# Optimization experiments

Hardware: AMD Instinct MI355X
Metric: run time of the kernel (lower is better)

The kernel has to match this reference:

```python
import jax, jax.numpy as jnp
import numpy as np

B, S, DIM, NH = 2, 2048, 1024, 8
DH = DIM // NH
GATE_SOFT_CAP = 15.0
BACKEND_EPS = 5e-05
NORM_EPS = 1e-06


def setup_inputs() -> dict:
    key = jax.random.key(0)
    kq, kk, kv, kw = jax.random.split(key, 4)
    q = jax.random.normal(kq, (B, S, DIM), dtype=jnp.float32)
    k = jax.random.normal(kk, (B, S, DIM), dtype=jnp.float32)
    v = jax.random.normal(kv, (B, S, DIM), dtype=jnp.float32)
    # ifgate: Linear(3*dim, 2*num_heads). Init weight is zeros in the module;
    # use small random weights so the gate path is non-trivial.
    ifgate_w = 0.02 * jax.random.normal(kw, (2 * NH, 3 * DIM), dtype=jnp.float32)
    # bias per reset_parameters: i_bias = -10, f_bias = linspace(3, 6, NH)
    ifgate_b = jnp.concatenate([
        jnp.full((NH,), -10.0, dtype=jnp.float32),
        jnp.linspace(3.0, 6.0, NH, dtype=jnp.float32),
    ])
    # residual-weight RMSNorm gain: effective gain = 1 + outnorm_w (init zeros)
    outnorm_w = jnp.zeros((DIM,), dtype=jnp.float32)
    return {"q": q, "k": k, "v": v, "ifgate_w": ifgate_w,
            "ifgate_b": ifgate_b, "outnorm_w": outnorm_w}


def _mlstm_parallel(q, k, v, i_pre, f_pre):
    # q,k,v: (B,NH,S,DH); i_pre,f_pre: (B,NH,S). Native stabilized parallel mLSTM.
    log_fg = jax.nn.log_sigmoid(f_pre)                       # (B,NH,S)
    lf_cs = jnp.cumsum(log_fg, axis=-1)                      # (B,NH,S)
    lf = jnp.concatenate([jnp.zeros_like(lf_cs[..., :1]), lf_cs], axis=-1)  # (B,NH,S+1)
    # log_D[t, s] = sum_{j=s+1}^{t} log_fg[j] + i_pre[s]  for s <= t, else -inf
    log_d = lf[..., 1:, None] - lf[..., None, 1:] + i_pre[..., None, :]     # (B,NH,S,S)
    t_idx = jnp.arange(q.shape[2])
    mask = t_idx[:, None] >= t_idx[None, :]
    log_d = jnp.where(mask, log_d, -jnp.inf)
    m = jnp.max(log_d, axis=-1, keepdims=True)               # (B,NH,S,1)
    d_mat = jnp.exp(log_d - m)                               # stabilized decays
    scores = jnp.einsum("bhtd,bhsd->bhts", q, k) * (1.0 / np.sqrt(DH))
    s_mat = scores * d_mat                                   # (B,NH,S,S)
    denom = jnp.maximum(jnp.abs(jnp.sum(s_mat, axis=-1, keepdims=True)),
                        jnp.exp(-m)) + BACKEND_EPS
    return jnp.einsum("bhts,bhsd->bhtd", s_mat, v) / denom   # (B,NH,S,DH)


def reference(q, k, v, ifgate_w, ifgate_b, outnorm_w):
    b, s, dim = q.shape
    # gate preactivations from concatenated q,k,v with tanh soft cap
    gate_in = jnp.concatenate([q, k, v], axis=-1)            # (B,S,3*DIM)
    pre = gate_in @ ifgate_w.T + ifgate_b                    # (B,S,2*NH)
    pre = GATE_SOFT_CAP * jnp.tanh(pre / GATE_SOFT_CAP)
    i_pre = pre[..., :NH].transpose(0, 2, 1)                 # (B,NH,S)
    f_pre = pre[..., NH:].transpose(0, 2, 1)                 # (B,NH,S)
    # split heads
    qh = q.reshape(b, s, NH, DH).transpose(0, 2, 1, 3)
    kh = k.reshape(b, s, NH, DH).transpose(0, 2, 1, 3)
    vh = v.reshape(b, s, NH, DH).transpose(0, 2, 1, 3)
    h = _mlstm_parallel(qh, kh, vh, i_pre, f_pre)            # (B,NH,S,DH)
    # multi-head RMSNorm with residual gain (bias is unused in the module's forward)
    rrms = jax.lax.rsqrt(jnp.mean(h * h, axis=-1, keepdims=True) + NORM_EPS)
    gain = (1.0 + outnorm_w).reshape(1, NH, 1, DH)
    h = h * rrms * gain
    return h.transpose(0, 2, 1, 3).reshape(b, s, dim)
```

## Files before the change

kernel.cpp:

```cpp
#include <hip/hip_runtime.h>
#include <math.h>

#define BB 2
#define SS 2048
#define DIMM 1024
#define NHH 8
#define DHH 128

constexpr float GATE_CAP = 15.0f;
constexpr float B_EPS = 5e-5f;
constexpr float N_EPS = 1e-6f;
constexpr float K_IS = 0.08838834764831845f;

typedef _Float16 f16x8 __attribute__((ext_vector_type(8)));
typedef __fp16  h16x2 __attribute__((ext_vector_type(2)));
typedef float f32x4 __attribute__((ext_vector_type(4)));

union U8 { f16x8 v; h16x2 h[4]; unsigned int u[4]; };

__device__ inline unsigned short f2bf(float x) {
    unsigned u = __builtin_bit_cast(unsigned, x);
    unsigned r = (u + 0x7fff + ((u >> 16) & 1)) >> 16;
    return (unsigned short)r;
}
__device__ inline float bf2f(unsigned short s) {
    unsigned u = ((unsigned)s) << 16;
    return __builtin_bit_cast(float, u);
}

#define GLD_LDS16(gsrc, ldst)                                                   \
    __builtin_amdgcn_global_load_lds(                                           \
        (const __attribute__((address_space(1))) unsigned int*)(gsrc),          \
        (__attribute__((address_space(3))) unsigned int*)(ldst), 16, 0, 0)

__global__ __launch_bounds__(256) void gate_kernel(
    const float* __restrict__ q, const float* __restrict__ k, const float* __restrict__ v,
    const float* __restrict__ gw, const float* __restrict__ gb,
    float* __restrict__ i_pre, float* __restrict__ lfcs)
{
    __shared__ __align__(16) float xs[2][8][1024];

    const int tid = threadIdx.x;
    const int lane = tid & 63;
    const int wv = tid >> 6;
    const int bs0 = blockIdx.x * 8;

    const float* srcs[3] = {q, k, v};

    auto stage = [&](int buf, int i) {
        const char* src = (const char*)(srcs[i] + (size_t)bs0 * DIMM);
        #pragma unroll
        for (int j = 0; j < 8; ++j) {
            GLD_LDS16(src + j * 4096 + wv * 1024 + lane * 16,
                      (char*)&xs[buf][j][0] + wv * 1024 + lane * 16);
        }
    };

    float acc[8][4];
    #pragma unroll
    for (int r = 0; r < 8; ++r)
        #pragma unroll
        for (int o = 0; o < 4; ++o) acc[r][o] = 0.f;

    stage(0, 0);

    for (int i = 0; i < 3; ++i) {
        const int cur = i & 1;
        if (i < 2) {
            stage(cur ^ 1, i + 1);
            asm volatile("s_waitcnt vmcnt(8)" ::: "memory");
        } else {
            asm volatile("s_waitcnt vmcnt(0)" ::: "memory");
        }
        __builtin_amdgcn_s_barrier();
        __builtin_amdgcn_sched_barrier(0);

        const float* gwi = gw + (wv * 4) * 3 * DIMM + i * DIMM;
        #pragma unroll
        for (int step = 0; step < 4; ++step) {
            float4 w4[4];
            #pragma unroll
            for (int o = 0; o < 4; ++o)
                w4[o] = *(const float4*)&gwi[o * 3 * DIMM + step * 256 + lane * 4];
            #pragma unroll
            for (int r = 0; r < 8; ++r) {
                const float4 xv = *(const float4*)&xs[cur][r][step * 256 + lane * 4];
                #pragma unroll
                for (int o = 0; o < 4; ++o)
                    acc[r][o] += xv.x * w4[o].x + xv.y * w4[o].y
                               + xv.z * w4[o].z + xv.w * w4[o].w;
            }
        }
        __builtin_amdgcn_s_barrier();
    }

    #pragma unroll
    for (int r = 0; r < 8; ++r)
        #pragma unroll
        for (int o = 0; o < 4; ++o) {
            acc[r][o] += __shfl_xor(acc[r][o], 16);
            acc[r][o] += __shfl_xor(acc[r][o], 32);
        }

    float* scr = &xs[0][0][0];
    const int l16 = lane & 15;
    if (l16 == lane) {
        #pragma unroll
        for (int r = 0; r < 8; ++r) {
            float4 st = {acc[r][0], acc[r][1], acc[r][2], acc[r][3]};
            *(float4*)&scr[wv * 576 + l16 * 36 + r * 4] = st;
        }
    }
    __syncthreads();

    if (tid < 128) {
        const int row = tid & 7, o = tid >> 3;
        const float* base = &scr[(o >> 2) * 576 + row * 4 + (o & 3)];
        float s = 0.f;
        #pragma unroll
        for (int j = 0; j < 16; ++j) s += base[j * 36];
        float p = s + gb[o];
        p = GATE_CAP * tanhf(p / GATE_CAP);
        const int bs = bs0 + row;
        const int b = bs >> 11, s2 = bs & 2047;
        if (o < NHH) {
            i_pre[((size_t)b * NHH + o) * SS + s2] = p;
        } else {
            const int h = o - NHH;
            const float ls = (p >= 0.f) ? -log1pf(expf(-p)) : p - log1pf(expf(p));
            lfcs[((size_t)b * NHH + h) * SS + s2] = ls;
        }
    }
}

__global__ __launch_bounds__(256) void prep_kv(
    const float* __restrict__ k, const float* __restrict__ v,
    unsigned short* __restrict__ k16, unsigned short* __restrict__ v16)
{
    const int id = blockIdx.x;
    const int bh = id & 15;
    const int st = id >> 4;
    const int b = bh >> 3, h = bh & 7;
    const int tid = threadIdx.x;

    {
        const float* kp = k + ((size_t)b * SS + st * 64) * DIMM + h * DHH;
        char* kb_ = (char*)k16 + ((size_t)bh * SS + st * 64) * 256;
        #pragma unroll
        for (int j = 0; j < 8; ++j) {
            const int item = j * 256 + tid;
            const int s = item >> 5, dq = item & 31;
            float4 kx = *(const float4*)&kp[(size_t)s * DIMM + dq * 4];
            h16x2 p0 = __builtin_amdgcn_cvt_pkrtz(kx.x, kx.y);
            h16x2 p1 = __builtin_amdgcn_cvt_pkrtz(kx.z, kx.w);
            uint2 wd;
            wd.x = __builtin_bit_cast(unsigned int, p0);
            wd.y = __builtin_bit_cast(unsigned int, p1);
            *(uint2*)(kb_ + s * 256 + ((dq * 8) ^ ((s & 7) << 4))) = wd;
        }
    }

    {
        const int d2 = (tid & 63) * 2;
        const int kb = (tid >> 6) & 1;
        const int gq = tid >> 7;
        const float* vp = v + ((size_t)b * SS + st * 64 + kb * 32) * DIMM + h * DHH + d2;
        char* base = (char*)v16 + ((size_t)bh * 32 + st) * 16384;
        #pragma unroll
        for (int gg = 0; gg < 2; ++gg) {
            const int g = gq * 2 + gg;
            float2 e[8];
            #pragma unroll
            for (int j = 0; j < 8; ++j) {
                const int s = 16 * (j >> 2) + 4 * g + (j & 3);
                e[j] = *(const float2*)&vp[(size_t)s * DIMM];
            }
            U8 u0, u1;
            u0.h[0] = __builtin_amdgcn_cvt_pkrtz(e[0].x, e[1].x);
            u0.h[1] = __builtin_amdgcn_cvt_pkrtz(e[2].x, e[3].x);
            u0.h[2] = __builtin_amdgcn_cvt_pkrtz(e[4].x, e[5].x);
            u0.h[3] = __builtin_amdgcn_cvt_pkrtz(e[6].x, e[7].x);
            u1.h[0] = __builtin_amdgcn_cvt_pkrtz(e[0].y, e[1].y);
            u1.h[1] = __builtin_amdgcn_cvt_pkrtz(e[2].y, e[3].y);
            u1.h[2] = __builtin_amdgcn_cvt_pkrtz(e[4].y, e[5].y);
            u1.h[3] = __builtin_amdgcn_cvt_pkrtz(e[6].y, e[7].y);
            const int p0 = kb * 64 + g * 16;
            *(f16x8*)(base + d2 * 128       + (p0 ^ ((d2 & 7) << 4)))       = u0.v;
            *(f16x8*)(base + (d2 + 1) * 128 + (p0 ^ (((d2 + 1) & 7) << 4))) = u1.v;
        }
    }
}

__global__ __launch_bounds__(256) void scan_kernel(
    const float* __restrict__ i_pre,
    float* __restrict__ lfcs, float* __restrict__ mstab, float* __restrict__ aa)
{
    const int bh = blockIdx.x;
    const int tid = threadIdx.x;
    const int lane = tid & 63, wv = tid >> 6;
    const size_t base = (size_t)bh * SS + tid * 8;

    float x[8];
    {
        float4 a0 = *(const float4*)&lfcs[base];
        float4 a1 = *(const float4*)&lfcs[base + 4];
        x[0] = a0.x; x[1] = a0.y; x[2] = a0.z; x[3] = a0.w;
        x[4] = a1.x; x[5] = a1.y; x[6] = a1.z; x[7] = a1.w;
    }
    #pragma unroll
    for (int i = 1; i < 8; ++i) x[i] += x[i - 1];

    const float tot = x[7];
    float inc = tot;
    #pragma unroll
    for (int off = 1; off < 64; off <<= 1) {
        float n = __shfl_up(inc, off);
        if (lane >= off) inc += n;
    }
    const float exc = inc - tot;

    __shared__ float wt[4], wm[4];
    if (lane == 63) wt[wv] = inc;
    __syncthreads();
    float wpre = 0.f;
    for (int w = 0; w < 4; ++w) if (w < wv) wpre += wt[w];
    const float off0 = exc + wpre;
    #pragma unroll
    for (int i = 0; i < 8; ++i) x[i] += off0;
    {
        float4 s0 = {x[0], x[1], x[2], x[3]}, s1 = {x[4], x[5], x[6], x[7]};
        *(float4*)&lfcs[base] = s0;
        *(float4*)&lfcs[base + 4] = s1;
    }

    float g[8];
    {
        float4 i0 = *(const float4*)&i_pre[base];
        float4 i1 = *(const float4*)&i_pre[base + 4];
        g[0] = i0.x - x[0]; g[1] = i0.y - x[1]; g[2] = i0.z - x[2]; g[3] = i0.w - x[3];
        g[4] = i1.x - x[4]; g[5] = i1.y - x[5]; g[6] = i1.z - x[6]; g[7] = i1.w - x[7];
        float4 s0 = {g[0], g[1], g[2], g[3]}, s1 = {g[4], g[5], g[6], g[7]};
        *(float4*)&aa[base] = s0;
        *(float4*)&aa[base + 4] = s1;
    }
    float mg[8];
    mg[0] = g[0];
    #pragma unroll
    for (int i = 1; i < 8; ++i) mg[i] = fmaxf(mg[i - 1], g[i]);

    float minc = mg[7];
    #pragma unroll
    for (int off = 1; off < 64; off <<= 1) {
        float n = __shfl_up(minc, off);
        if (lane >= off) minc = fmaxf(minc, n);
    }
    float mexc = __shfl_up(minc, 1);
    if (lane == 0) mexc = -1e30f;
    if (lane == 63) wm[wv] = minc;
    __syncthreads();
    float wmpre = -1e30f;
    for (int w = 0; w < 4; ++w) if (w < wv) wmpre = fmaxf(wmpre, wm[w]);
    const float pm = fmaxf(mexc, wmpre);
    float4 s0, s1;
    s0.x = x[0] + fmaxf(pm, mg[0]); s0.y = x[1] + fmaxf(pm, mg[1]);
    s0.z = x[2] + fmaxf(pm, mg[2]); s0.w = x[3] + fmaxf(pm, mg[3]);
    s1.x = x[4] + fmaxf(pm, mg[4]); s1.y = x[5] + fmaxf(pm, mg[5]);
    s1.z = x[6] + fmaxf(pm, mg[6]); s1.w = x[7] + fmaxf(pm, mg[7]);
    *(float4*)&mstab[base] = s0;
    *(float4*)&mstab[base + 4] = s1;
}

__global__ __launch_bounds__(256, 2) void mlstm_splitk(
    const float* __restrict__ q,
    const unsigned short* __restrict__ k16, const unsigned short* __restrict__ v16,
    const float* __restrict__ lfcs, const float* __restrict__ aa,
    unsigned short* __restrict__ pnum, float* __restrict__ pden)
{
    __shared__ __align__(16) unsigned short kbuf[2][8192];
    __shared__ __align__(16) unsigned short vbuf[2][8192];

    const int tid = threadIdx.x;
    const int lane = tid & 63;
    const int wv = tid >> 6;
    const int g = lane >> 4;
    const int l16 = lane & 15;

    const int id = blockIdx.x;
    int bh, qq, chunk;
    if (id < 256) {
        bh = id & 15;
        const int j = id >> 4;
        if (j < 7)       { qq = 5 + j;               chunk = 0; }
        else if (j == 7) { qq = 11;                  chunk = 1; }
        else             { qq = 12 + ((j - 8) >> 1); chunk = (j - 8) & 1; }
    } else {
        const int e = id - 256;
        bh = e & 15;
        const int j = e >> 4;
        if (j < 5)       { qq = j;             chunk = 0; }
        else if (j < 10) { qq = 6 + (j - 5);   chunk = 1; }
        else             { qq = 12 + (j - 10); chunk = 2; }
    }
    const int b = bh >> 3, h = bh & 7;
    const int tw0 = qq * 128 + 32 * wv;

    const size_t bhS = (size_t)bh * SS;
    const float* qp = q + (size_t)b * SS * DIMM + h * DHH;
    const char* kg = (const char*)k16 + (size_t)bh * 524288;
    const char* vg = (const char*)v16 + (size_t)bh * 524288;

    f16x8 qf[2][4];
    float cdec[2];
    #pragma unroll
    for (int nt = 0; nt < 2; ++nt) {
        const int t = tw0 + 16 * nt + l16;
        cdec[nt] = lfcs[bhS + t];
        const float* qrow = qp + (size_t)t * DIMM;
        #pragma unroll
        for (int kb = 0; kb < 4; ++kb) {
            float4 x0 = *(const float4*)&qrow[kb * 32 + g * 8];
            float4 x1 = *(const float4*)&qrow[kb * 32 + g * 8 + 4];
            U8 uu;
            uu.h[0] = __builtin_amdgcn_cvt_pkrtz(x0.x, x0.y);
            uu.h[1] = __builtin_amdgcn_cvt_pkrtz(x0.z, x0.w);
            uu.h[2] = __builtin_amdgcn_cvt_pkrtz(x1.x, x1.y);
            uu.h[3] = __builtin_amdgcn_cvt_pkrtz(x1.z, x1.w);
            qf[nt][kb] = uu.v;
        }
    }

    f32x4 oacc[2][8];
    #pragma unroll
    for (int nt = 0; nt < 2; ++nt)
        #pragma unroll
        for (int mt = 0; mt < 8; ++mt)
            oacc[nt][mt] = (f32x4){0.f, 0.f, 0.f, 0.f};
    float dpart[2] = {0.f, 0.f};

    const int st0 = chunk * 12;
    const int st1m = 2 * qq + 1;
    const int st1 = (st0 + 11 < st1m) ? (st0 + 11) : st1m;

    auto stage = [&](int bi, int st) {
        const char* ksrc = kg + (size_t)st * 16384;
        const char* vsrc = vg + (size_t)st * 16384;
        #pragma unroll
        for (int j = 0; j < 4; ++j) {
            const int off = (j * 4 + wv) * 1024;
            GLD_LDS16(ksrc + off + lane * 16, (char*)&kbuf[bi][0] + off);
            GLD_LDS16(vsrc + off + lane * 16, (char*)&vbuf[bi][0] + off);
        }
    };

    stage(0, st0);

    for (int st = st0; st <= st1; ++st) {
        const int cur = (st - st0) & 1;
        if (st < st1) {
            stage(cur ^ 1, st + 1);
            asm volatile("s_waitcnt vmcnt(8)" ::: "memory");
        } else {
            asm volatile("s_waitcnt vmcnt(0)" ::: "memory");
        }
        __builtin_amdgcn_s_barrier();
        __builtin_amdgcn_sched_barrier(0);

        const int s0 = st * 64;
        const float* ap = aa + bhS + s0;
        f32x4 av[4];
        av[0] = *(const f32x4*)&ap[g * 4];
        av[1] = *(const f32x4*)&ap[16 + g * 4];
        av[2] = *(const f32x4*)&ap[32 + g * 4];
        av[3] = *(const f32x4*)&ap[48 + g * 4];

        f32x4 stacc[2][4];
        #pragma unroll
        for (int nt = 0; nt < 2; ++nt)
            #pragma unroll
            for (int ct = 0; ct < 4; ++ct)
                stacc[nt][ct] = (f32x4){0.f, 0.f, 0.f, 0.f};
        #pragma unroll
        for (int ct = 0; ct < 4; ++ct) {
            const int row = ct * 16 + l16;
            #pragma unroll
            for (int kb = 0; kb < 4; ++kb) {
                f16x8 kf = *(const f16x8*)((const char*)&kbuf[cur][0] +
                            ((row * 256 + kb * 64 + g * 16) ^ ((row & 7) << 4)));
                stacc[0][ct] = __builtin_amdgcn_mfma_f32_16x16x32_f16(kf, qf[0][kb], stacc[0][ct], 0, 0, 0);
                stacc[1][ct] = __builtin_amdgcn_mfma_f32_16x16x32_f16(kf, qf[1][kb], stacc[1][ct], 0, 0, 0);
            }
        }

        const bool diag = (st >= 2 * qq);
        #pragma unroll
        for (int nt = 0; nt < 2; ++nt) {
            float dsum = 0.f;
            const int t_idx = tw0 + nt * 16 + l16;
            #pragma unroll
            for (int ct = 0; ct < 4; ++ct) {
                #pragma unroll
                for (int i = 0; i < 4; ++i) {
                    const float e = K_IS * __expf(cdec[nt] + av[ct][i]);
                    float val = stacc[nt][ct][i] * e;
                    if (diag && (s0 + ct * 16 + g * 4 + i > t_idx)) val = 0.f;
                    dsum += val;
                    stacc[nt][ct][i] = val;
                }
            }
            dpart[nt] += dsum;
        }

        f16x8 pf[2][2];
        #pragma unroll
        for (int nt = 0; nt < 2; ++nt) {
            #pragma unroll
            for (int kb = 0; kb < 2; ++kb) {
                U8 uu;
                uu.h[0] = __builtin_amdgcn_cvt_pkrtz(stacc[nt][2 * kb][0],     stacc[nt][2 * kb][1]);
                uu.h[1] = __builtin_amdgcn_cvt_pkrtz(stacc[nt][2 * kb][2],     stacc[nt][2 * kb][3]);
                uu.h[2] = __builtin_amdgcn_cvt_pkrtz(stacc[nt][2 * kb + 1][0], stacc[nt][2 * kb + 1][1]);
                uu.h[3] = __builtin_amdgcn_cvt_pkrtz(stacc[nt][2 * kb + 1][2], stacc[nt][2 * kb + 1][3]);
                pf[nt][kb] = uu.v;
            }
        }

        #pragma unroll
        for (int mt = 0; mt < 8; ++mt) {
            const int dI = mt * 16 + l16;
            #pragma unroll
            for (int kb = 0; kb < 2; ++kb) {
                f16x8 vf = *(const f16x8*)((const char*)&vbuf[cur][0] +
                            dI * 128 + ((kb * 64 + g * 16) ^ ((dI & 7) << 4)));
                oacc[0][mt] = __builtin_amdgcn_mfma_f32_16x16x32_f16(vf, pf[0][kb], oacc[0][mt], 0, 0, 0);
                oacc[1][mt] = __builtin_amdgcn_mfma_f32_16x16x32_f16(vf, pf[1][kb], oacc[1][mt], 0, 0, 0);
            }
        }
        __builtin_amdgcn_sched_barrier(0);
        __builtin_amdgcn_s_barrier();
    }

    const int uoff = (qq < 6) ? qq : ((qq < 12) ? (6 + 2 * (qq - 6)) : (18 + 3 * (qq - 12)));
    const size_t cidx = (size_t)bh * 30 + uoff + chunk;
    #pragma unroll
    for (int nt = 0; nt < 2; ++nt) {
        float den = dpart[nt];
        den += __shfl_xor(den, 16);
        den += __shfl_xor(den, 32);
        const int row = wv * 32 + nt * 16 + l16;
        if (g == 0) pden[cidx * 128 + row] = den;
        #pragma unroll
        for (int mt = 0; mt < 8; ++mt) {
            ushort4 pk;
            pk.x = f2bf(oacc[nt][mt][0]);
            pk.y = f2bf(oacc[nt][mt][1]);
            pk.z = f2bf(oacc[nt][mt][2]);
            pk.w = f2bf(oacc[nt][mt][3]);
            *(ushort4*)&pnum[((cidx * 64 + wv * 16 + nt * 8 + mt) << 8) + lane * 4] = pk;
        }
    }
}

__global__ __launch_bounds__(256) void reduce_kernel(
    const unsigned short* __restrict__ pnum, const float* __restrict__ pden,
    const float* __restrict__ mstab, const float* __restrict__ onw,
    float* __restrict__ out)
{
    const int id = blockIdx.x;
    const int bh = id & 15;
    const int qq = id >> 4;
    const int b = bh >> 3, h = bh & 7;
    const int tid = threadIdx.x;
    const int lane = tid & 63;
    const int wv = tid >> 6;
    const int g = lane >> 4;
    const int l16 = lane & 15;

    const int nch = (qq < 6) ? 1 : ((qq < 12) ? 2 : 3);
    const int uoff = (qq < 6) ? qq : ((qq < 12) ? (6 + 2 * (qq - 6)) : (18 + 3 * (qq - 12)));
    const size_t cbase = (size_t)bh * 30 + uoff;

    f32x4 acc[2][8];
    #pragma unroll
    for (int nt = 0; nt < 2; ++nt)
        #pragma unroll
        for (int mt = 0; mt < 8; ++mt)
            acc[nt][mt] = (f32x4){0.f, 0.f, 0.f, 0.f};
    float den[2] = {0.f, 0.f};

    for (int c = 0; c < nch; ++c) {
        const size_t fb = (cbase + c) * 64 + wv * 16;
        #pragma unroll
        for (int nt = 0; nt < 2; ++nt) {
            #pragma unroll
            for (int mt = 0; mt < 8; ++mt) {
                ushort4 t4 = *(const ushort4*)&pnum[((fb + nt * 8 + mt) << 8) + lane * 4];
                acc[nt][mt][0] += bf2f(t4.x);
                acc[nt][mt][1] += bf2f(t4.y);
                acc[nt][mt][2] += bf2f(t4.z);
                acc[nt][mt][3] += bf2f(t4.w);
            }
            den[nt] += pden[(cbase + c) * 128 + wv * 32 + nt * 16 + l16];
        }
    }

    #pragma unroll
    for (int nt = 0; nt < 2; ++nt) {
        const int t = qq * 128 + wv * 32 + nt * 16 + l16;
        const float m = mstab[(size_t)bh * SS + t];
        const float em = __expf(-m);
        const float dt = den[nt] * em;
        const float denf = fmaxf(fabsf(dt), em) + B_EPS;
        const float inv = em / denf;
        float ssq = 0.f;
        #pragma unroll
        for (int mt = 0; mt < 8; ++mt) {
            #pragma unroll
            for (int i = 0; i < 4; ++i) {
                acc[nt][mt][i] *= inv;
                ssq += acc[nt][mt][i] * acc[nt][mt][i];
            }
        }
        ssq += __shfl_xor(ssq, 16);
        ssq += __shfl_xor(ssq, 32);
        const float rms = rsqrtf(ssq * (1.0f / DHH) + N_EPS);

        float* orow = out + ((size_t)b * SS + t) * DIMM + h * DHH;
        #pragma unroll
        for (int mt = 0; mt < 8; ++mt) {
            float4 gn = *(const float4*)&onw[h * DHH + mt * 16 + g * 4];
            float4 o4;
            o4.x = acc[nt][mt][0] * rms * (1.f + gn.x);
            o4.y = acc[nt][mt][1] * rms * (1.f + gn.y);
            o4.z = acc[nt][mt][2] * rms * (1.f + gn.z);
            o4.w = acc[nt][mt][3] * rms * (1.f + gn.w);
            *(float4*)&orow[mt * 16 + g * 4] = o4;
        }
    }
}

extern "C" void kernel_launch(void* const* d_in, const int* in_sizes, int n_in,
                              void* d_out, int out_size, void* d_ws, size_t ws_size,
                              hipStream_t stream) {
    const float* q   = (const float*)d_in[0];
    const float* k   = (const float*)d_in[1];
    const float* v   = (const float*)d_in[2];
    const float* gw  = (const float*)d_in[3];
    const float* gb  = (const float*)d_in[4];
    const float* onw = (const float*)d_in[5];
    float* out = (float*)d_out;

    float* ws    = (float*)d_ws;
    float* i_pre = ws;
    float* lfcs  = ws + 32768;
    float* mm    = ws + 65536;
    float* aa    = ws + 98304;
    float* pden  = ws + 131072;
    unsigned short* pnum = (unsigned short*)((char*)d_ws + 1048576);
    unsigned short* k16  = (unsigned short*)((char*)d_ws + 16777216);
    unsigned short* v16  = (unsigned short*)((char*)d_ws + 25165824);

    hipLaunchKernelGGL(gate_kernel, dim3(BB * SS / 8), dim3(256), 0, stream,
                       q, k, v, gw, gb, i_pre, lfcs);
    hipLaunchKernelGGL(prep_kv, dim3(16 * 32), dim3(256), 0, stream, k, v, k16, v16);
    hipLaunchKernelGGL(scan_kernel, dim3(BB * NHH), dim3(256), 0, stream, i_pre, lfcs, mm, aa);
    hipLaunchKernelGGL(mlstm_splitk, dim3(480), dim3(256), 0, stream,
                       q, k16, v16, lfcs, aa, pnum, pden);
    hipLaunchKernelGGL(reduce_kernel, dim3(16 * 16), dim3(256), 0, stream,
                       pnum, pden, mm, onw, out);
}
```

Baseline: 84.07 us.

## Fuse prep and scan kernels, interleave QK/PV MFMA phases, use exp2 decay

Merges the K/V fp16 conversion kernel and the gate scan kernel into one launch, with the extra blocks doing the scan, which removes one launch boundary. In the mLSTM split-K kernel, the QK^T, decay and PV stages are split into halves and interleaved, with s_setprio raised around the MFMA sections, so matrix and vector work can overlap. The decay exponent is precomputed in base-2 with the 1/sqrt(d) scale folded into the log, so exp2 replaces expf times a constant. The gate weights and the decay-vector loads are hoisted ahead of the barrier waits to hide their latency, at the cost of more live registers.

```diff
diff --git a/kernel.cpp b/kernel.cpp
--- a/kernel.cpp
+++ b/kernel.cpp
@@ -10,7 +10,8 @@
 constexpr float GATE_CAP = 15.0f;
 constexpr float B_EPS = 5e-5f;
 constexpr float N_EPS = 1e-6f;
-constexpr float K_IS = 0.08838834764831845f;
+constexpr float LOG2E = 1.4426950408889634f;
+constexpr float LN_KIS = -2.4260151319598084f;
 
 typedef _Float16 f16x8 __attribute__((ext_vector_type(8)));
 typedef __fp16  h16x2 __attribute__((ext_vector_type(2)));
@@ -66,6 +67,14 @@
 
     for (int i = 0; i < 3; ++i) {
         const int cur = i & 1;
+        const float* gwi = gw + (wv * 4) * 3 * DIMM + i * DIMM;
+        float4 w4[4][4];
+        #pragma unroll
+        for (int step = 0; step < 4; ++step)
+            #pragma unroll
+            for (int o = 0; o < 4; ++o)
+                w4[step][o] = *(const float4*)&gwi[o * 3 * DIMM + step * 256 + lane * 4];
+
         if (i < 2) {
             stage(cur ^ 1, i + 1);
             asm volatile("s_waitcnt vmcnt(8)" ::: "memory");
@@ -75,20 +84,15 @@
         __builtin_amdgcn_s_barrier();
         __builtin_amdgcn_sched_barrier(0);
 
-        const float* gwi = gw + (wv * 4) * 3 * DIMM + i * DIMM;
         #pragma unroll
         for (int step = 0; step < 4; ++step) {
-            float4 w4[4];
-            #pragma unroll
-            for (int o = 0; o < 4; ++o)
-                w4[o] = *(const float4*)&gwi[o * 3 * DIMM + step * 256 + lane * 4];
             #pragma unroll
             for (int r = 0; r < 8; ++r) {
                 const float4 xv = *(const float4*)&xs[cur][r][step * 256 + lane * 4];
                 #pragma unroll
                 for (int o = 0; o < 4; ++o)
-                    acc[r][o] += xv.x * w4[o].x + xv.y * w4[o].y
-                               + xv.z * w4[o].z + xv.w * w4[o].w;
+                    acc[r][o] += xv.x * w4[step][o].x + xv.y * w4[step][o].y
+                               + xv.z * w4[step][o].z + xv.w * w4[step][o].w;
             }
         }
         __builtin_amdgcn_s_barrier();
@@ -133,70 +137,70 @@
     }
 }
 
-__global__ __launch_bounds__(256) void prep_kv(
+__global__ __launch_bounds__(256) void prep_scan(
     const float* __restrict__ k, const float* __restrict__ v,
-    unsigned short* __restrict__ k16, unsigned short* __restrict__ v16)
-{
-    const int id = blockIdx.x;
-    const int bh = id & 15;
-    const int st = id >> 4;
-    const int b = bh >> 3, h = bh & 7;
-    const int tid = threadIdx.x;
-
-    {
-        const float* kp = k + ((size_t)b * SS + st * 64) * DIMM + h * DHH;
-        char* kb_ = (char*)k16 + ((size_t)bh * SS + st * 64) * 256;
-        #pragma unroll
-        for (int j = 0; j < 8; ++j) {
-            const int item = j * 256 + tid;
-            const int s = item >> 5, dq = item & 31;
-            float4 kx = *(const float4*)&kp[(size_t)s * DIMM + dq * 4];
-            h16x2 p0 = __builtin_amdgcn_cvt_pkrtz(kx.x, kx.y);
-            h16x2 p1 = __builtin_amdgcn_cvt_pkrtz(kx.z, kx.w);
-            uint2 wd;
-            wd.x = __builtin_bit_cast(unsigned int, p0);
-            wd.y = __builtin_bit_cast(unsigned int, p1);
-            *(uint2*)(kb_ + s * 256 + ((dq * 8) ^ ((s & 7) << 4))) = wd;
-        }
-    }
-
-    {
-        const int d2 = (tid & 63) * 2;
-        const int kb = (tid >> 6) & 1;
-        const int gq = tid >> 7;
-        const float* vp = v + ((size_t)b * SS + st * 64 + kb * 32) * DIMM + h * DHH + d2;
-        char* base = (char*)v16 + ((size_t)bh * 32 + st) * 16384;
-        #pragma unroll
-        for (int gg = 0; gg < 2; ++gg) {
-            const int g = gq * 2 + gg;
-            float2 e[8];
-            #pragma unroll
-            for (int j = 0; j < 8; ++j) {
-                const int s = 16 * (j >> 2) + 4 * g + (j & 3);
-                e[j] = *(const float2*)&vp[(size_t)s * DIMM];
-            }
-            U8 u0, u1;
-            u0.h[0] = __builtin_amdgcn_cvt_pkrtz(e[0].x, e[1].x);
-            u0.h[1] = __builtin_amdgcn_cvt_pkrtz(e[2].x, e[3].x);
-            u0.h[2] = __builtin_amdgcn_cvt_pkrtz(e[4].x, e[5].x);
-            u0.h[3] = __builtin_amdgcn_cvt_pkrtz(e[6].x, e[7].x);
-            u1.h[0] = __builtin_amdgcn_cvt_pkrtz(e[0].y, e[1].y);
-            u1.h[1] = __builtin_amdgcn_cvt_pkrtz(e[2].y, e[3].y);
-            u1.h[2] = __builtin_amdgcn_cvt_pkrtz(e[4].y, e[5].y);
-            u1.h[3] = __builtin_amdgcn_cvt_pkrtz(e[6].y, e[7].y);
-            const int p0 = kb * 64 + g * 16;
-            *(f16x8*)(base + d2 * 128       + (p0 ^ ((d2 & 7) << 4)))       = u0.v;
-            *(f16x8*)(base + (d2 + 1) * 128 + (p0 ^ (((d2 + 1) & 7) << 4))) = u1.v;
-        }
-    }
-}
-
-__global__ __launch_bounds__(256) void scan_kernel(
+    unsigned short* __restrict__ k16, unsigned short* __restrict__ v16,
     const float* __restrict__ i_pre,
     float* __restrict__ lfcs, float* __restrict__ mstab, float* __restrict__ aa)
 {
-    const int bh = blockIdx.x;
+    const int id = blockIdx.x;
     const int tid = threadIdx.x;
+    __shared__ float wt[4], wm[4];
+
+    if (id < 512) {
+        const int bh = id & 15;
+        const int st = id >> 4;
+        const int b = bh >> 3, h = bh & 7;
+
+        {
+            const float* kp = k + ((size_t)b * SS + st * 64) * DIMM + h * DHH;
+            char* kb_ = (char*)k16 + ((size_t)bh * SS + st * 64) * 256;
+            #pragma unroll
+            for (int j = 0; j < 8; ++j) {
+                const int item = j * 256 + tid;
+                const int s = item >> 5, dq = item & 31;
+                float4 kx = *(const float4*)&kp[(size_t)s * DIMM + dq * 4];
+                h16x2 p0 = __builtin_amdgcn_cvt_pkrtz(kx.x, kx.y);
+                h16x2 p1 = __builtin_amdgcn_cvt_pkrtz(kx.z, kx.w);
+                uint2 wd;
+                wd.x = __builtin_bit_cast(unsigned int, p0);
+                wd.y = __builtin_bit_cast(unsigned int, p1);
+                *(uint2*)(kb_ + s * 256 + ((dq * 8) ^ ((s & 7) << 4))) = wd;
+            }
+        }
+        {
+            const int d2 = (tid & 63) * 2;
+            const int kb = (tid >> 6) & 1;
+            const int gq = tid >> 7;
+            const float* vp = v + ((size_t)b * SS + st * 64 + kb * 32) * DIMM + h * DHH + d2;
+            char* base = (char*)v16 + ((size_t)bh * 32 + st) * 16384;
+            #pragma unroll
+            for (int gg = 0; gg < 2; ++gg) {
+                const int g = gq * 2 + gg;
+                float2 e[8];
+                #pragma unroll
+                for (int j = 0; j < 8; ++j) {
+                    const int s = 16 * (j >> 2) + 4 * g + (j & 3);
+                    e[j] = *(const float2*)&vp[(size_t)s * DIMM];
+                }
+                U8 u0, u1;
+                u0.h[0] = __builtin_amdgcn_cvt_pkrtz(e[0].x, e[1].x);
+                u0.h[1] = __builtin_amdgcn_cvt_pkrtz(e[2].x, e[3].x);
+                u0.h[2] = __builtin_amdgcn_cvt_pkrtz(e[4].x, e[5].x);
+                u0.h[3] = __builtin_amdgcn_cvt_pkrtz(e[6].x, e[7].x);
+                u1.h[0] = __builtin_amdgcn_cvt_pkrtz(e[0].y, e[1].y);
+                u1.h[1] = __builtin_amdgcn_cvt_pkrtz(e[2].y, e[3].y);
+                u1.h[2] = __builtin_amdgcn_cvt_pkrtz(e[4].y, e[5].y);
+                u1.h[3] = __builtin_amdgcn_cvt_pkrtz(e[6].y, e[7].y);
+                const int p0 = kb * 64 + g * 16;
+                *(f16x8*)(base + d2 * 128       + (p0 ^ ((d2 & 7) << 4)))       = u0.v;
+                *(f16x8*)(base + (d2 + 1) * 128 + (p0 ^ (((d2 + 1) & 7) << 4))) = u1.v;
+            }
+        }
+        return;
+    }
+
+    const int bh = id - 512;
     const int lane = tid & 63, wv = tid >> 6;
     const size_t base = (size_t)bh * SS + tid * 8;
 
@@ -219,7 +223,6 @@
     }
     const float exc = inc - tot;
 
-    __shared__ float wt[4], wm[4];
     if (lane == 63) wt[wv] = inc;
     __syncthreads();
     float wpre = 0.f;
@@ -239,7 +242,8 @@
         float4 i1 = *(const float4*)&i_pre[base + 4];
         g[0] = i0.x - x[0]; g[1] = i0.y - x[1]; g[2] = i0.z - x[2]; g[3] = i0.w - x[3];
         g[4] = i1.x - x[4]; g[5] = i1.y - x[5]; g[6] = i1.z - x[6]; g[7] = i1.w - x[7];
-        float4 s0 = {g[0], g[1], g[2], g[3]}, s1 = {g[4], g[5], g[6], g[7]};
+        float4 s0 = {g[0] * LOG2E, g[1] * LOG2E, g[2] * LOG2E, g[3] * LOG2E};
+        float4 s1 = {g[4] * LOG2E, g[5] * LOG2E, g[6] * LOG2E, g[7] * LOG2E};
         *(float4*)&aa[base] = s0;
         *(float4*)&aa[base + 4] = s1;
     }
@@ -310,11 +314,11 @@
     const char* vg = (const char*)v16 + (size_t)bh * 524288;
 
     f16x8 qf[2][4];
-    float cdec[2];
+    float cdec2[2];
     #pragma unroll
     for (int nt = 0; nt < 2; ++nt) {
         const int t = tw0 + 16 * nt + l16;
-        cdec[nt] = lfcs[bhS + t];
+        cdec2[nt] = (lfcs[bhS + t] + LN_KIS) * LOG2E;
         const float* qrow = qp + (size_t)t * DIMM;
         #pragma unroll
         for (int kb = 0; kb < 4; ++kb) {
@@ -356,6 +360,13 @@
 
     for (int st = st0; st <= st1; ++st) {
         const int cur = (st - st0) & 1;
+        const float* ap = aa + bhS + st * 64;
+        f32x4 av[4];
+        av[0] = *(const f32x4*)&ap[g * 4];
+        av[1] = *(const f32x4*)&ap[16 + g * 4];
+        av[2] = *(const f32x4*)&ap[32 + g * 4];
+        av[3] = *(const f32x4*)&ap[48 + g * 4];
+
         if (st < st1) {
             stage(cur ^ 1, st + 1);
             asm volatile("s_waitcnt vmcnt(8)" ::: "memory");
@@ -366,12 +377,7 @@
         __builtin_amdgcn_sched_barrier(0);
 
         const int s0 = st * 64;
-        const float* ap = aa + bhS + s0;
-        f32x4 av[4];
-        av[0] = *(const f32x4*)&ap[g * 4];
-        av[1] = *(const f32x4*)&ap[16 + g * 4];
-        av[2] = *(const f32x4*)&ap[32 + g * 4];
-        av[3] = *(const f32x4*)&ap[48 + g * 4];
+        const bool diag = (st >= 2 * qq);
 
         f32x4 stacc[2][4];
         #pragma unroll
@@ -379,62 +385,72 @@
             #pragma unroll
             for (int ct = 0; ct < 4; ++ct)
                 stacc[nt][ct] = (f32x4){0.f, 0.f, 0.f, 0.f};
-        #pragma unroll
-        for (int ct = 0; ct < 4; ++ct) {
-            const int row = ct * 16 + l16;
-            #pragma unroll
-            for (int kb = 0; kb < 4; ++kb) {
-                f16x8 kf = *(const f16x8*)((const char*)&kbuf[cur][0] +
-                            ((row * 256 + kb * 64 + g * 16) ^ ((row & 7) << 4)));
-                stacc[0][ct] = __builtin_amdgcn_mfma_f32_16x16x32_f16(kf, qf[0][kb], stacc[0][ct], 0, 0, 0);
-                stacc[1][ct] = __builtin_amdgcn_mfma_f32_16x16x32_f16(kf, qf[1][kb], stacc[1][ct], 0, 0, 0);
+
+        f16x8 pf[2][2];
+
+        #define QKT_PAIR(CT0)                                                            \
+            __builtin_amdgcn_s_setprio(1);                                               \
+            _Pragma("unroll")                                                            \
+            for (int ct = CT0; ct < CT0 + 2; ++ct) {                                     \
+                const int row = ct * 16 + l16;                                           \
+                _Pragma("unroll")                                                        \
+                for (int kb = 0; kb < 4; ++kb) {                                         \
+                    f16x8 kf = *(const f16x8*)((const char*)&kbuf[cur][0] +              \
+                                ((row * 256 + kb * 64 + g * 16) ^ ((row & 7) << 4)));    \
+                    stacc[0][ct] = __builtin_amdgcn_mfma_f32_16x16x32_f16(kf, qf[0][kb], stacc[0][ct], 0, 0, 0); \
+                    stacc[1][ct] = __builtin_amdgcn_mfma_f32_16x16x32_f16(kf, qf[1][kb], stacc[1][ct], 0, 0, 0); \
+                }                                                                        \
+            }                                                                            \
+            __builtin_amdgcn_s_setprio(0);
+
+        #define DECAY_PACK(KB)                                                           \
+            _Pragma("unroll")                                                            \
+            for (int nt = 0; nt < 2; ++nt) {                                             \
+                float dsum = 0.f;                                                        \
+                const int t_idx = tw0 + nt * 16 + l16;                                   \
+                _Pragma("unroll")                                                        \
+                for (int ct = 2 * (KB); ct < 2 * (KB) + 2; ++ct) {                       \
+                    _Pragma("unroll")                                                    \
+                    for (int i = 0; i < 4; ++i) {                                        \
+                        const float e = __builtin_amdgcn_exp2f(cdec2[nt] + av[ct][i]);   \
+                        float val = stacc[nt][ct][i] * e;                                \
+                        if (diag && (s0 + ct * 16 + g * 4 + i > t_idx)) val = 0.f;       \
+                        dsum += val;                                                     \
+                        stacc[nt][ct][i] = val;                                          \
+                    }                                                                    \
+                }                                                                        \
+                dpart[nt] += dsum;                                                       \
+                U8 uu;                                                                   \
+                uu.h[0] = __builtin_amdgcn_cvt_pkrtz(stacc[nt][2*(KB)][0],   stacc[nt][2*(KB)][1]);   \
+                uu.h[1] = __builtin_amdgcn_cvt_pkrtz(stacc[nt][2*(KB)][2],   stacc[nt][2*(KB)][3]);   \
+                uu.h[2] = __builtin_amdgcn_cvt_pkrtz(stacc[nt][2*(KB)+1][0], stacc[nt][2*(KB)+1][1]); \
+                uu.h[3] = __builtin_amdgcn_cvt_pkrtz(stacc[nt][2*(KB)+1][2], stacc[nt][2*(KB)+1][3]); \
+                pf[nt][KB] = uu.v;                                                       \
             }
-        }
-
-        const bool diag = (st >= 2 * qq);
-        #pragma unroll
-        for (int nt = 0; nt < 2; ++nt) {
-            float dsum = 0.f;
-            const int t_idx = tw0 + nt * 16 + l16;
-            #pragma unroll
-            for (int ct = 0; ct < 4; ++ct) {
-                #pragma unroll
-                for (int i = 0; i < 4; ++i) {
-                    const float e = K_IS * __expf(cdec[nt] + av[ct][i]);
-                    float val = stacc[nt][ct][i] * e;
-                    if (diag && (s0 + ct * 16 + g * 4 + i > t_idx)) val = 0.f;
-                    dsum += val;
-                    stacc[nt][ct][i] = val;
-                }
-            }
-            dpart[nt] += dsum;
-        }
-
-        f16x8 pf[2][2];
-        #pragma unroll
-        for (int nt = 0; nt < 2; ++nt) {
-            #pragma unroll
-            for (int kb = 0; kb < 2; ++kb) {
-                U8 uu;
-                uu.h[0] = __builtin_amdgcn_cvt_pkrtz(stacc[nt][2 * kb][0],     stacc[nt][2 * kb][1]);
-                uu.h[1] = __builtin_amdgcn_cvt_pkrtz(stacc[nt][2 * kb][2],     stacc[nt][2 * kb][3]);
-                uu.h[2] = __builtin_amdgcn_cvt_pkrtz(stacc[nt][2 * kb + 1][0], stacc[nt][2 * kb + 1][1]);
-                uu.h[3] = __builtin_amdgcn_cvt_pkrtz(stacc[nt][2 * kb + 1][2], stacc[nt][2 * kb + 1][3]);
-                pf[nt][kb] = uu.v;
-            }
-        }
-
-        #pragma unroll
-        for (int mt = 0; mt < 8; ++mt) {
-            const int dI = mt * 16 + l16;
-            #pragma unroll
-            for (int kb = 0; kb < 2; ++kb) {
-                f16x8 vf = *(const f16x8*)((const char*)&vbuf[cur][0] +
-                            dI * 128 + ((kb * 64 + g * 16) ^ ((dI & 7) << 4)));
-                oacc[0][mt] = __builtin_amdgcn_mfma_f32_16x16x32_f16(vf, pf[0][kb], oacc[0][mt], 0, 0, 0);
-                oacc[1][mt] = __builtin_amdgcn_mfma_f32_16x16x32_f16(vf, pf[1][kb], oacc[1][mt], 0, 0, 0);
-            }
-        }
+
+        #define PV_HALF(KB)                                                              \
+            __builtin_amdgcn_s_setprio(1);                                               \
+            _Pragma("unroll")                                                            \
+            for (int mt = 0; mt < 8; ++mt) {                                             \
+                const int dI = mt * 16 + l16;                                            \
+                f16x8 vf = *(const f16x8*)((const char*)&vbuf[cur][0] +                  \
+                            dI * 128 + (((KB) * 64 + g * 16) ^ ((dI & 7) << 4)));        \
+                oacc[0][mt] = __builtin_amdgcn_mfma_f32_16x16x32_f16(vf, pf[0][KB], oacc[0][mt], 0, 0, 0); \
+                oacc[1][mt] = __builtin_amdgcn_mfma_f32_16x16x32_f16(vf, pf[1][KB], oacc[1][mt], 0, 0, 0); \
+            }                                                                            \
+            __builtin_amdgcn_s_setprio(0);
+
+        QKT_PAIR(0)
+        DECAY_PACK(0)
+        QKT_PAIR(2)
+        PV_HALF(0)
+        DECAY_PACK(1)
+        PV_HALF(1)
+
+        #undef QKT_PAIR
+        #undef DECAY_PACK
+        #undef PV_HALF
+
         __builtin_amdgcn_sched_barrier(0);
         __builtin_amdgcn_s_barrier();
     }
@@ -561,8 +577,8 @@
 
     hipLaunchKernelGGL(gate_kernel, dim3(BB * SS / 8), dim3(256), 0, stream,
                        q, k, v, gw, gb, i_pre, lfcs);
-    hipLaunchKernelGGL(prep_kv, dim3(16 * 32), dim3(256), 0, stream, k, v, k16, v16);
-    hipLaunchKernelGGL(scan_kernel, dim3(BB * NHH), dim3(256), 0, stream, i_pre, lfcs, mm, aa);
+    hipLaunchKernelGGL(prep_scan, dim3(528), dim3(256), 0, stream,
+                       k, v, k16, v16, i_pre, lfcs, mm, aa);
     hipLaunchKernelGGL(mlstm_splitk, dim3(480), dim3(256), 0, stream,
                        q, k16, v16, lfcs, aa, pnum, pden);
     hipLaunchKernelGGL(reduce_kernel, dim3(16 * 16), dim3(256), 0, stream,
```

New measurement: 80.35 us. -4.4%, faster.
